# Optimization experiments

Hardware: AMD Instinct MI355X
Metric: run time of the kernel (lower is better)

Reference implementation:

```python
import jax, jax.numpy as jnp
import numpy as np

B, T, IN_CH, FIRST_CH, BLOCK_CH, SCALED_CH, K, ND = 8, 16384, 256, 256, 24, 128, 2, 10


def _conv1d(x, W, b, d=1):
    # x: (B, L, Cin), W: (K, Cin, Cout), keras Conv1D with padding='valid'
    y = jax.lax.conv_general_dilated(x, W, (1,), 'VALID', rhs_dilation=(d,),
                                     dimension_numbers=('NWC', 'WIO', 'NWC'))
    return y + b


def _gated(x, gW, gb, fW, fb, sW, sb, d):
    g = jax.nn.sigmoid(_conv1d(x, gW, gb, d))
    f = jnp.tanh(_conv1d(x, fW, fb, d))
    return _conv1d(f * g, sW, sb, 1)


def setup_inputs():
    key = jax.random.key(0)
    ks = jax.random.split(key, 11)
    s = 0.1
    n9 = ND - 1  # blocks 1..9 share channel count BLOCK_CH -> stacked weights
    return {
        'x': jax.random.normal(ks[0], (B, T, IN_CH), jnp.float32),
        'causal_W': jax.random.normal(ks[1], (K, IN_CH, FIRST_CH)) * s,
        'causal_b': jnp.zeros((FIRST_CH,)),
        'gW0': jax.random.normal(ks[2], (K, FIRST_CH, BLOCK_CH)) * s,
        'gb0': jnp.zeros((BLOCK_CH,)),
        'fW0': jax.random.normal(ks[3], (K, FIRST_CH, BLOCK_CH)) * s,
        'fb0': jnp.zeros((BLOCK_CH,)),
        'sW0': jax.random.normal(ks[4], (1, BLOCK_CH, BLOCK_CH)) * s,
        'sb0': jnp.zeros((BLOCK_CH,)),
        'gate_W': jax.random.normal(ks[5], (n9, K, BLOCK_CH, BLOCK_CH)) * s,
        'gate_b': jnp.zeros((n9, BLOCK_CH)),
        'filter_W': jax.random.normal(ks[6], (n9, K, BLOCK_CH, BLOCK_CH)) * s,
        'filter_b': jnp.zeros((n9, BLOCK_CH)),
        'scale_W': jax.random.normal(ks[7], (n9, 1, BLOCK_CH, BLOCK_CH)) * s,
        'scale_b': jnp.zeros((n9, BLOCK_CH)),
        'res_W': jax.random.normal(ks[8], (n9, 1, BLOCK_CH, SCALED_CH)) * s,
        'res_b': jnp.zeros((n9, SCALED_CH)),
        'f1_W': jax.random.normal(ks[9], (1, SCALED_CH, IN_CH)) * s,
        'f1_b': jnp.zeros((IN_CH,)),
        'f2_W': jax.random.normal(ks[10], (1, IN_CH, IN_CH)) * s,
        'f2_b': jnp.zeros((IN_CH,)),
    }


def reference(x, causal_W, causal_b, gW0, gb0, fW0, fb0, sW0, sb0,
              gate_W, gate_b, filter_W, filter_b, scale_W, scale_b,
              res_W, res_b, f1_W, f1_b, f2_W, f2_b):
    out = _conv1d(x, causal_W, causal_b)  # (B, T-1, 256)
    # block 0 (dilation 1): prev_in has 256 ch vs 24 ch out -> residual branch skipped
    out = _gated(out, gW0, gb0, fW0, fb0, sW0, sb0, 1)
    acc = None
    for i in range(ND - 1):
        d = 2 ** (i + 1)  # even -> trim d//2 on each side
        prev = out
        out = _gated(prev, gate_W[i], gate_b[i], filter_W[i], filter_b[i],
                     scale_W[i], scale_b[i], d)
        trimmed = prev[:, d // 2: prev.shape[1] - d // 2, :]
        # NOTE: original code OVERWRITES the accumulator each iteration
        acc = _conv1d(trimmed + out, res_W[i], res_b[i], 1)
    a = jax.nn.relu(acc)  # (B, 15360, 128)
    a = jax.nn.relu(_conv1d(a, f1_W, f1_b, 1))  # (B, 15360, 256)
    return jax.nn.softmax(_conv1d(a, f2_W, f2_b, 1), axis=-1)
```

## Files before the change

kernel.cpp:

```cpp
#include <hip/hip_runtime.h>
#include <math.h>

typedef unsigned short u16;
typedef __attribute__((ext_vector_type(8))) short short8;
typedef __attribute__((ext_vector_type(4))) float f32x4;

#define PBSTR ((long)16382 * 24)

__device__ __forceinline__ u16 f2bf(float f) {
    unsigned u = __float_as_uint(f);
    unsigned r = u + 0x7FFFu + ((u >> 16) & 1u);
    return (u16)(r >> 16);
}
__device__ __forceinline__ float bf2f(u16 v) { return __uint_as_float((unsigned)v << 16); }
__device__ __forceinline__ float sigf(float x) { return 1.f / (1.f + __expf(-x)); }
__device__ __forceinline__ float tanhfast(float x) { return 2.f / (1.f + __expf(-2.f * x)) - 1.f; }

__device__ __forceinline__ unsigned cvtpk(float a, float b) {
    unsigned r;
    asm("v_cvt_pk_bf16_f32 %0, %1, %2" : "=v"(r) : "v"(a), "v"(b));
    return r;
}
__device__ __forceinline__ short8 ldfrag8(const float* p) {
    float4 v0 = *(const float4*)p;
    float4 v1 = *(const float4*)(p + 4);
    union { uint4 u; short8 s; } cv;
    cv.u.x = cvtpk(v0.x, v0.y); cv.u.y = cvtpk(v0.z, v0.w);
    cv.u.z = cvtpk(v1.x, v1.y); cv.u.w = cvtpk(v1.z, v1.w);
    return cv.s;
}

__global__ __launch_bounds__(256) void build_all(
    const float* __restrict__ cW, const float* __restrict__ cb,
    const float* __restrict__ gW, const float* __restrict__ gb,
    const float* __restrict__ fW, const float* __restrict__ fb,
    u16* __restrict__ Wt, float* __restrict__ biasGF,
    const float* __restrict__ f1W, const float* __restrict__ f2W,
    const float* __restrict__ resW8,
    const float* __restrict__ gateW, const float* __restrict__ filtW,
    const float* __restrict__ sclW, const float* __restrict__ s0W,
    u16* __restrict__ Wt1, u16* __restrict__ Wt2, u16* __restrict__ Wtr,
    u16* __restrict__ Wgf, u16* __restrict__ Wsc)
{
    if (blockIdx.x < 192) {
        int idx = blockIdx.x * 256 + threadIdx.x;
        if (idx < 49152) {
            int nr = idx / 768, k = idx % 768, tau = k / 256, ci = k % 256;
            float val = 0.f;
            if (nr < 48) {
                const float* G = (nr < 24) ? gW : fW;
                int n = (nr < 24) ? nr : nr - 24;
                auto dotf = [&](int i, int j) {
                    const float* a = cW + i * 65536 + ci * 256;
                    const float* g = G + j * 6144 + n;
                    float s = 0.f;
                    for (int o = 0; o < 256; o += 4) {
                        float4 av = *(const float4*)(a + o);
                        const float* gp = g + o * 24;
                        s += av.x * gp[0] + av.y * gp[24] + av.z * gp[48] + av.w * gp[72];
                    }
                    return s;
                };
                if (tau == 0)      val = dotf(0, 0);
                else if (tau == 1) val = dotf(0, 1) + dotf(1, 0);
                else               val = dotf(1, 1);
            }
            Wt[idx] = f2bf(val);
        }
        if (blockIdx.x == 0 && threadIdx.x < 48) {
            int nr = threadIdx.x;
            const float* G = (nr < 24) ? gW : fW;
            const float* B = (nr < 24) ? gb : fb;
            int n = (nr < 24) ? nr : nr - 24;
            float s = B[n];
            for (int o = 0; o < 256; ++o) s += cb[o] * (G[o * 24 + n] + G[6144 + o * 24 + n]);
            biasGF[nr] = s;
        }
    } else {
        int idx = (blockIdx.x - 192) * 256 + threadIdx.x;
        if (idx < 32768) {
            int n = idx / 128, k = idx % 128;
            Wt1[idx] = f2bf(f1W[k * 256 + n]);
        } else if (idx < 98304) {
            int j = idx - 32768; int n = j / 256, k = j % 256;
            Wt2[j] = f2bf(f2W[k * 256 + n]);
        } else if (idx < 102400) {
            int j = idx - 98304; int n = j / 32, k = j % 32;
            Wtr[j] = (k < 24) ? f2bf(resW8[k * 128 + n]) : (u16)0;
        } else if (idx < 130048) {
            int j = idx - 102400;
            int i = j / 3072, r = (j % 3072) / 64, k = j % 64;
            float v = 0.f;
            int tap = -1, ci = 0;
            if (k < 24) { tap = 0; ci = k; }
            else if (k >= 32 && k < 56) { tap = 1; ci = k - 32; }
            if (tap >= 0) {
                const float* W = (r < 24) ? gateW : filtW;
                int co = (r < 24) ? r : r - 24;
                v = W[((i * 2 + tap) * 24 + ci) * 24 + co];
            }
            Wgf[j] = f2bf(v);
        } else if (idx < 140288) {
            int j = idx - 130048;
            int i = j / 1024, r = (j % 1024) / 32, k = j % 32;
            const float* S = (i < 9) ? (sclW + (size_t)i * 576) : s0W;
            float v = (r < 24 && k < 24) ? S[k * 24 + r] : 0.f;
            Wsc[j] = f2bf(v);
        }
    }
}

__global__ __launch_bounds__(256) void gf_fused_v6(
    const float* __restrict__ x, const u16* __restrict__ Wt,
    const float* __restrict__ biasGF,
    const u16* __restrict__ ws0, const float* __restrict__ sb,
    u16* __restrict__ P)
{
    __shared__ __align__(16) union {
        u16 bs[48 * 776];
        u16 H[256 * 40];
    } U;

    const int tid = threadIdx.x;
    const int m0 = blockIdx.x * 256;
    const int b = blockIdx.z;
    const float* xb = x + (long)b * (16384 * 256);

    for (int i = tid; i < 4608; i += 256) {
        int rn = i / 96, kk = i % 96;
        *(uint4*)&U.bs[rn * 776 + kk * 8] = *(const uint4*)(Wt + (long)rn * 768 + kk * 8);
    }

    const int wv = tid >> 6, lane = tid & 63, col = lane & 15, quad = lane >> 4;

    short8 wsf0 = *(const short8*)(ws0 + col * 32 + quad * 8);
    short8 wsf1 = *(const short8*)(ws0 + (16 + col) * 32 + quad * 8);
    const float bv0 = biasGF[col];
    const float bv1 = (col < 8) ? biasGF[16 + col] : biasGF[24 + col - 8];
    const float bv2 = biasGF[32 + col];
    const float sv0 = sb[col];
    const float sv1 = (col < 8) ? sb[16 + col] : 0.f;

    long rowoff[4];
#pragma unroll
    for (int mt = 0; mt < 4; ++mt) {
        int g = m0 + wv * 64 + mt * 16 + col;
        if (g > 16381) g = 16381;
        rowoff[mt] = (long)g * 256 + quad * 8;
    }

    f32x4 acc[4][3];
#pragma unroll
    for (int i = 0; i < 4; ++i)
#pragma unroll
        for (int j = 0; j < 3; ++j) acc[i][j] = (f32x4){0.f, 0.f, 0.f, 0.f};

    __syncthreads();

    for (int s = 0; s < 24; ++s) {
        short8 a[4];
#pragma unroll
        for (int mt = 0; mt < 4; ++mt)
            a[mt] = ldfrag8(xb + rowoff[mt] + s * 32);
#pragma unroll
        for (int nt = 0; nt < 3; ++nt) {
            short8 bb = *(const short8*)&U.bs[(nt * 16 + col) * 776 + s * 32 + quad * 8];
#pragma unroll
            for (int mt = 0; mt < 4; ++mt)
                acc[mt][nt] = __builtin_amdgcn_mfma_f32_16x16x32_bf16(a[mt], bb, acc[mt][nt], 0, 0, 0);
        }
    }

    __syncthreads();
    *(uint4*)&U.H[tid * 40 + 24] = (uint4){0, 0, 0, 0};

#pragma unroll
    for (int mt = 0; mt < 4; ++mt) {
        const int lr = wv * 64 + mt * 16 + quad * 4;
#pragma unroll
        for (int rr = 0; rr < 4; ++rr) {
            float g0 = acc[mt][0][rr] + bv0;
            float m1 = acc[mt][1][rr] + bv1;
            float m2 = acc[mt][2][rr] + bv2;
            float s1 = __shfl_xor(m1, 8);
            float s2 = __shfl_xor(m2, 8);
            float f0 = (col < 8) ? s1 : s2;
            U.H[(lr + rr) * 40 + col] = f2bf(sigf(g0) * tanhfast(f0));
            if (col < 8)
                U.H[(lr + rr) * 40 + 16 + col] = f2bf(sigf(m1) * tanhfast(s2));
        }
    }
    __syncthreads();

#pragma unroll
    for (int mt = 0; mt < 4; ++mt) {
        short8 aH = *(const short8*)&U.H[(wv * 64 + mt * 16 + col) * 40 + quad * 8];
        f32x4 c0 = {0.f, 0.f, 0.f, 0.f}, c1 = c0;
        c0 = __builtin_amdgcn_mfma_f32_16x16x32_bf16(aH, wsf0, c0, 0, 0, 0);
        c1 = __builtin_amdgcn_mfma_f32_16x16x32_bf16(aH, wsf1, c1, 0, 0, 0);
#pragma unroll
        for (int rr = 0; rr < 4; ++rr) {
            int t = m0 + wv * 64 + mt * 16 + quad * 4 + rr;
            if (t < 16382) {
                P[(long)b * PBSTR + (long)t * 24 + col] = f2bf(c0[rr] + sv0);
                if (col < 8)
                    P[(long)b * PBSTR + (long)t * 24 + 16 + col] = f2bf(c1[rr] + sv1);
            }
        }
    }
}

__global__ __launch_bounds__(256) void gated_mfma_v3(
    const u16* __restrict__ Pin,
    const u16* __restrict__ wg,
    const u16* __restrict__ ws,
    const float* __restrict__ gB, const float* __restrict__ fB,
    const float* __restrict__ sB,
    u16* __restrict__ Q, int Lout, int d, int trimOff)
{
    __shared__ __align__(16) u16 T[128 * 72];
    __shared__ __align__(16) u16 H[128 * 40];

    const int tid = threadIdx.x;
    const int wv = tid >> 6, lane = tid & 63, col = lane & 15, quad = lane >> 4;
    const int m0 = blockIdx.x * 128;
    const int b = blockIdx.z;
    const u16* Pb = Pin + (long)b * PBSTR;

    {
        int r = tid & 127, tap = tid >> 7;
        int t = m0 + r; if (t > Lout - 1) t = Lout - 1;
        const u16* src = Pb + (long)(t + tap * d) * 24;
        u16* dst = &T[r * 72 + tap * 32];
        *(uint4*)(dst)      = *(const uint4*)(src);
        *(uint4*)(dst + 8)  = *(const uint4*)(src + 8);
        *(uint4*)(dst + 16) = *(const uint4*)(src + 16);
        *(uint4*)(dst + 24) = (uint4){0, 0, 0, 0};
    }
    if (tid < 128) *(uint4*)&H[tid * 40 + 24] = (uint4){0, 0, 0, 0};

    short8 bgf0[3], bgf1[3];
#pragma unroll
    for (int nt = 0; nt < 3; ++nt) {
        bgf0[nt] = *(const short8*)(wg + (nt * 16 + col) * 64 + quad * 8);
        bgf1[nt] = *(const short8*)(wg + (nt * 16 + col) * 64 + 32 + quad * 8);
    }
    short8 wsf0 = *(const short8*)(ws + col * 32 + quad * 8);
    short8 wsf1 = *(const short8*)(ws + (16 + col) * 32 + quad * 8);
    const float bv0 = gB[col];
    const float bv1 = (col < 8) ? gB[16 + col] : fB[col - 8];
    const float bv2 = fB[8 + col];
    const float sv0 = sB[col];
    const float sv1 = (col < 8) ? sB[16 + col] : 0.f;

    __syncthreads();

#pragma unroll
    for (int mt = 0; mt < 2; ++mt) {
        const int r = wv * 32 + mt * 16;
        short8 a0 = *(const short8*)&T[(r + col) * 72 + quad * 8];
        short8 a1 = *(const short8*)&T[(r + col) * 72 + 32 + quad * 8];
        f32x4 ac0 = {0.f, 0.f, 0.f, 0.f}, ac1 = ac0, ac2 = ac0;
        ac0 = __builtin_amdgcn_mfma_f32_16x16x32_bf16(a0, bgf0[0], ac0, 0, 0, 0);
        ac0 = __builtin_amdgcn_mfma_f32_16x16x32_bf16(a1, bgf1[0], ac0, 0, 0, 0);
        ac1 = __builtin_amdgcn_mfma_f32_16x16x32_bf16(a0, bgf0[1], ac1, 0, 0, 0);
        ac1 = __builtin_amdgcn_mfma_f32_16x16x32_bf16(a1, bgf1[1], ac1, 0, 0, 0);
        ac2 = __builtin_amdgcn_mfma_f32_16x16x32_bf16(a0, bgf0[2], ac2, 0, 0, 0);
        ac2 = __builtin_amdgcn_mfma_f32_16x16x32_bf16(a1, bgf1[2], ac2, 0, 0, 0);

        const int lr = r + quad * 4;
#pragma unroll
        for (int rr = 0; rr < 4; ++rr) {
            float g0 = ac0[rr] + bv0;
            float m1 = ac1[rr] + bv1;
            float m2 = ac2[rr] + bv2;
            float s1 = __shfl_xor(m1, 8);
            float s2 = __shfl_xor(m2, 8);
            float f0 = (col < 8) ? s1 : s2;
            H[(lr + rr) * 40 + col] = f2bf(sigf(g0) * tanhfast(f0));
            if (col < 8)
                H[(lr + rr) * 40 + 16 + col] = f2bf(sigf(m1) * tanhfast(s2));
        }
    }
    __syncthreads();

#pragma unroll
    for (int mt = 0; mt < 2; ++mt) {
        short8 aH = *(const short8*)&H[(wv * 32 + mt * 16 + col) * 40 + quad * 8];
        f32x4 c0 = {0.f, 0.f, 0.f, 0.f}, c1 = c0;
        c0 = __builtin_amdgcn_mfma_f32_16x16x32_bf16(aH, wsf0, c0, 0, 0, 0);
        c1 = __builtin_amdgcn_mfma_f32_16x16x32_bf16(aH, wsf1, c1, 0, 0, 0);
#pragma unroll
        for (int rr = 0; rr < 4; ++rr) {
            int t = m0 + wv * 32 + mt * 16 + quad * 4 + rr;
            if (t < Lout) {
                float v0 = c0[rr] + sv0;
                if (trimOff >= 0) v0 += bf2f(Pb[(long)(t + trimOff) * 24 + col]);
                Q[(long)b * PBSTR + (long)t * 24 + col] = f2bf(v0);
                if (col < 8) {
                    float v1 = c1[rr] + sv1;
                    if (trimOff >= 0) v1 += bf2f(Pb[(long)(t + trimOff) * 24 + 16 + col]);
                    Q[(long)b * PBSTR + (long)t * 24 + 16 + col] = f2bf(v1);
                }
            }
        }
    }
}

__global__ __launch_bounds__(256) void res_f1_fused(
    const u16* __restrict__ Pfin,
    const u16* __restrict__ Wtr, const float* __restrict__ resb,
    const u16* __restrict__ Wt1, const float* __restrict__ f1b,
    u16* __restrict__ A1)
{
    __shared__ __align__(16) u16 ACCs[128 * 136];
    __shared__ __align__(16) u16 W1s[128 * 136];
    __shared__ float biasL[128];

    const int tid = threadIdx.x;
    const int wv = tid >> 6, lane = tid & 63, col = lane & 15, quad = lane >> 4;
    const int b = blockIdx.z;
    const int n0 = blockIdx.y * 128;
    const int m0 = blockIdx.x * 128;
    const u16* Pb = Pfin + (long)b * PBSTR;

    for (int i = tid; i < 2048; i += 256) {
        int rn = i >> 4, kk = i & 15;
        *(uint4*)&W1s[rn * 136 + kk * 8] = *(const uint4*)(Wt1 + (long)(n0 + rn) * 128 + kk * 8);
    }
    if (tid < 128) biasL[tid] = f1b[n0 + tid];

    short8 bfr[8];
    float rbv[8];
#pragma unroll
    for (int nt = 0; nt < 8; ++nt) {
        bfr[nt] = *(const short8*)(Wtr + (nt * 16 + col) * 32 + quad * 8);
        rbv[nt] = resb[nt * 16 + col];
    }
    short8 afr[2];
#pragma unroll
    for (int mt = 0; mt < 2; ++mt) {
        int r = m0 + wv * 32 + mt * 16 + col;
        if (r > 15359) r = 15359;
        afr[mt] = *(const short8*)(Pb + (long)r * 24 + quad * 8);
    }
    f32x4 acc[2][8];
#pragma unroll
    for (int i = 0; i < 2; ++i)
#pragma unroll
        for (int j = 0; j < 8; ++j) acc[i][j] = (f32x4){0.f, 0.f, 0.f, 0.f};
#pragma unroll
    for (int nt = 0; nt < 8; ++nt) {
        acc[0][nt] = __builtin_amdgcn_mfma_f32_16x16x32_bf16(afr[0], bfr[nt], acc[0][nt], 0, 0, 0);
        acc[1][nt] = __builtin_amdgcn_mfma_f32_16x16x32_bf16(afr[1], bfr[nt], acc[1][nt], 0, 0, 0);
    }
#pragma unroll
    for (int mt = 0; mt < 2; ++mt)
#pragma unroll
        for (int nt = 0; nt < 8; ++nt)
#pragma unroll
            for (int rr = 0; rr < 4; ++rr) {
                int lrow = wv * 32 + mt * 16 + quad * 4 + rr;
                ACCs[lrow * 136 + nt * 16 + col] = f2bf(fmaxf(acc[mt][nt][rr] + rbv[nt], 0.f));
            }
    __syncthreads();

    f32x4 acc2[2][8];
#pragma unroll
    for (int i = 0; i < 2; ++i)
#pragma unroll
        for (int j = 0; j < 8; ++j) acc2[i][j] = (f32x4){0.f, 0.f, 0.f, 0.f};
#pragma unroll
    for (int ks = 0; ks < 4; ++ks) {
        short8 am[2];
#pragma unroll
        for (int mt = 0; mt < 2; ++mt)
            am[mt] = *(const short8*)&ACCs[(wv * 32 + mt * 16 + col) * 136 + ks * 32 + quad * 8];
#pragma unroll
        for (int nt = 0; nt < 8; ++nt) {
            short8 bb = *(const short8*)&W1s[(nt * 16 + col) * 136 + ks * 32 + quad * 8];
            acc2[0][nt] = __builtin_amdgcn_mfma_f32_16x16x32_bf16(am[0], bb, acc2[0][nt], 0, 0, 0);
            acc2[1][nt] = __builtin_amdgcn_mfma_f32_16x16x32_bf16(am[1], bb, acc2[1][nt], 0, 0, 0);
        }
    }
#pragma unroll
    for (int mt = 0; mt < 2; ++mt)
#pragma unroll
        for (int nt = 0; nt < 8; ++nt)
#pragma unroll
            for (int rr = 0; rr < 4; ++rr) {
                int t = m0 + wv * 32 + mt * 16 + quad * 4 + rr;
                float v = fmaxf(acc2[mt][nt][rr] + biasL[nt * 16 + col], 0.f);
                A1[((long)b * 15360 + t) * 256 + n0 + nt * 16 + col] = f2bf(v);
            }
}

__global__ __launch_bounds__(256) void f2_softmax_v2(
    const u16* __restrict__ A, const u16* __restrict__ Wt2,
    const float* __restrict__ bias, float* __restrict__ out)
{
    __shared__ __align__(16) u16 Bs[2][256 * 40];
    __shared__ float biasL[256];
    const int tid = threadIdx.x;
    const int b = blockIdx.y;
    const int t0 = blockIdx.x * 64;
    biasL[tid] = bias[tid];

    const int wv = tid >> 6, lane = tid & 63, col = lane & 15, quad = lane >> 4;
    const u16* Ab = A + (long)b * (15360L * 256);
    const int row = t0 + wv * 16 + col;

    auto stage = [&](int kc, int buf) {
#pragma unroll
        for (int j = 0; j < 4; ++j) {
            int idx = tid * 4 + j;
            int rn = idx >> 2, kk = idx & 3;
            *(uint4*)&Bs[buf][rn * 40 + kk * 8] =
                *(const uint4*)(Wt2 + (long)rn * 256 + kc * 32 + kk * 8);
        }
    };

    short8 afr[8];
#pragma unroll
    for (int kc = 0; kc < 8; ++kc)
        afr[kc] = *(const short8*)(Ab + (long)row * 256 + kc * 32 + quad * 8);

    f32x4 acc[16];
#pragma unroll
    for (int i = 0; i < 16; ++i) acc[i] = (f32x4){0.f, 0.f, 0.f, 0.f};

    stage(0, 0);
    __syncthreads();
    for (int kc = 0; kc < 8; ++kc) {
        int buf = kc & 1;
        if (kc < 7) stage(kc + 1, buf ^ 1);
#pragma unroll
        for (int nt = 0; nt < 16; ++nt) {
            short8 bb = *(const short8*)&Bs[buf][(nt * 16 + col) * 40 + quad * 8];
            acc[nt] = __builtin_amdgcn_mfma_f32_16x16x32_bf16(afr[kc], bb, acc[nt], 0, 0, 0);
        }
        __syncthreads();
    }

#pragma unroll
    for (int r = 0; r < 4; ++r) {
        int tl = wv * 16 + quad * 4 + r;
        float v[16];
        float m = -1e30f;
#pragma unroll
        for (int nt = 0; nt < 16; ++nt) {
            v[nt] = acc[nt][r] + biasL[nt * 16 + col];
            m = fmaxf(m, v[nt]);
        }
        m = fmaxf(m, __shfl_xor(m, 1));
        m = fmaxf(m, __shfl_xor(m, 2));
        m = fmaxf(m, __shfl_xor(m, 4));
        m = fmaxf(m, __shfl_xor(m, 8));
        float s = 0.f;
#pragma unroll
        for (int nt = 0; nt < 16; ++nt) { v[nt] = __expf(v[nt] - m); s += v[nt]; }
        s += __shfl_xor(s, 1);
        s += __shfl_xor(s, 2);
        s += __shfl_xor(s, 4);
        s += __shfl_xor(s, 8);
        float inv = 1.f / s;
        float* op = out + ((long)b * 15360 + t0 + tl) * 256;
#pragma unroll
        for (int nt = 0; nt < 16; ++nt) op[nt * 16 + col] = v[nt] * inv;
    }
}

extern "C" void kernel_launch(void* const* d_in, const int* in_sizes, int n_in,
                              void* d_out, int out_size, void* d_ws, size_t ws_size,
                              hipStream_t stream)
{
    const float* x        = (const float*)d_in[0];
    const float* causal_W = (const float*)d_in[1];
    const float* causal_b = (const float*)d_in[2];
    const float* gW0      = (const float*)d_in[3];
    const float* gb0      = (const float*)d_in[4];
    const float* fW0      = (const float*)d_in[5];
    const float* fb0      = (const float*)d_in[6];
    const float* sW0      = (const float*)d_in[7];
    const float* sb0      = (const float*)d_in[8];
    const float* gate_W   = (const float*)d_in[9];
    const float* gate_b   = (const float*)d_in[10];
    const float* filter_W = (const float*)d_in[11];
    const float* filter_b = (const float*)d_in[12];
    const float* scale_W  = (const float*)d_in[13];
    const float* scale_b  = (const float*)d_in[14];
    const float* res_W    = (const float*)d_in[15];
    const float* res_b    = (const float*)d_in[16];
    const float* f1_W     = (const float*)d_in[17];
    const float* f1_b     = (const float*)d_in[18];
    const float* f2_W     = (const float*)d_in[19];
    const float* f2_b     = (const float*)d_in[20];

    char* w = (char*)d_ws;
    u16* A1   = (u16*)w;   w += (size_t)8 * 15360 * 256 * 2;
    u16* P0   = (u16*)w;   w += (size_t)8 * 16382 * 24 * 2 + 128;
    u16* P1   = (u16*)w;   w += (size_t)8 * 16382 * 24 * 2 + 128;
    u16* WtGF = (u16*)w;   w += (size_t)64 * 768 * 2;
    u16* Wt1  = (u16*)w;   w += (size_t)256 * 128 * 2;
    u16* Wt2  = (u16*)w;   w += (size_t)256 * 256 * 2;
    u16* Wtr  = (u16*)w;   w += (size_t)128 * 32 * 2;
    float* biasGF = (float*)w; w += 256;
    u16* WgfG = (u16*)w;   w += (size_t)9 * 48 * 64 * 2;
    u16* WsG  = (u16*)w;   w += (size_t)10 * 32 * 32 * 2;

    dim3 blk(256);

    build_all<<<dim3(740), blk, 0, stream>>>(
        causal_W, causal_b, gW0, gb0, fW0, fb0, WtGF, biasGF,
        f1_W, f2_W, res_W + (size_t)8 * 24 * 128,
        gate_W, filter_W, scale_W, sW0,
        Wt1, Wt2, Wtr, WgfG, WsG);

    gf_fused_v6<<<dim3(64, 1, 8), blk, 0, stream>>>(
        x, WtGF, biasGF, WsG + (size_t)9 * 1024, sb0, P0);

    u16* Pprev = P0;
    u16* Pnext = P1;
    int Lprev = 16382;
    for (int i = 0; i < 9; ++i) {
        int d = 2 << i;
        int L = Lprev - d;
        int trim = (i == 8) ? d / 2 : -1;
        gated_mfma_v3<<<dim3((L + 127) / 128, 1, 8), blk, 0, stream>>>(
            Pprev, WgfG + (size_t)i * 3072, WsG + (size_t)i * 1024,
            gate_b + i * 24, filter_b + i * 24, scale_b + i * 24,
            Pnext, L, d, trim);
        u16* tmp = Pprev; Pprev = Pnext; Pnext = tmp;
        Lprev = L;
    }

    res_f1_fused<<<dim3(120, 2, 8), blk, 0, stream>>>(
        Pprev, Wtr, res_b + 8 * 128, Wt1, f1_b, A1);

    f2_softmax_v2<<<dim3(240, 8), blk, 0, stream>>>(A1, Wt2, f2_b, (float*)d_out);
}
```

Before: 546.7 us.

## Double-buffer x tiles into LDS via async global_load_lds in first fused kernel

The first fused conv+gated kernel now stages 128-row fp32 x tiles into LDS with asynchronous global_load_lds, double-buffered and XOR-swizzled, instead of each lane loading its A fragments straight from global memory. The block tile is halved from 256 to 128 rows, doubling the grid, and the weight slab is loaded in two halves to shrink LDS. The aim is to overlap the large x read with MFMA work and raise occupancy. In exchange it adds a barrier per K step and a mid-loop weight reload, and each row's data is now fetched through LDS rather than held in registers.

```diff
diff --git a/kernel.cpp b/kernel.cpp
--- a/kernel.cpp
+++ b/kernel.cpp
@@ -28,6 +28,12 @@
     cv.u.x = cvtpk(v0.x, v0.y); cv.u.y = cvtpk(v0.z, v0.w);
     cv.u.z = cvtpk(v1.x, v1.y); cv.u.w = cvtpk(v1.z, v1.w);
     return cv.s;
+}
+
+__device__ __forceinline__ void gload16(const float* g, float* l) {
+    __builtin_amdgcn_global_load_lds(
+        (const __attribute__((address_space(1))) unsigned int*)g,
+        (__attribute__((address_space(3))) unsigned int*)l, 16, 0, 0);
 }
 
 __global__ __launch_bounds__(256) void build_all(
@@ -110,28 +116,45 @@
     }
 }
 
-__global__ __launch_bounds__(256) void gf_fused_v6(
+__global__ __launch_bounds__(256) void gf_fused_v7(
     const float* __restrict__ x, const u16* __restrict__ Wt,
     const float* __restrict__ biasGF,
     const u16* __restrict__ ws0, const float* __restrict__ sb,
     u16* __restrict__ P)
 {
     __shared__ __align__(16) union {
-        u16 bs[48 * 776];
-        u16 H[256 * 40];
+        u16 bs[48 * 392];
+        u16 H[128 * 40];
     } U;
+    __shared__ __align__(16) float ab[2][128 * 32];
 
     const int tid = threadIdx.x;
-    const int m0 = blockIdx.x * 256;
+    const int wv = tid >> 6, lane = tid & 63, col = lane & 15, quad = lane >> 4;
+    const int m0 = blockIdx.x * 128;
     const int b = blockIdx.z;
     const float* xb = x + (long)b * (16384 * 256);
 
-    for (int i = tid; i < 4608; i += 256) {
-        int rn = i / 96, kk = i % 96;
-        *(uint4*)&U.bs[rn * 776 + kk * 8] = *(const uint4*)(Wt + (long)rn * 768 + kk * 8);
-    }
-
-    const int wv = tid >> 6, lane = tid & 63, col = lane & 15, quad = lane >> 4;
+    long srcoff[4];
+#pragma unroll
+    for (int j = 0; j < 4; ++j) {
+        int lin = j * 256 + tid;
+        int rl = lin >> 3;
+        int r = m0 + rl;
+        if (r > 16381) r = 16381;
+        int ii = (lin & 7) ^ (rl & 7);
+        srcoff[j] = (long)r * 256 + ii * 4;
+    }
+
+    auto stageA = [&](int ks, int bufi) {
+#pragma unroll
+        for (int j = 0; j < 4; ++j)
+            gload16(xb + srcoff[j] + ks * 32, &ab[bufi][j * 1024 + wv * 256]);
+    };
+
+    for (int i = tid; i < 2304; i += 256) {
+        int rn = i / 48, kk = i % 48;
+        *(uint4*)&U.bs[rn * 392 + kk * 8] = *(const uint4*)(Wt + (long)rn * 768 + kk * 8);
+    }
 
     short8 wsf0 = *(const short8*)(ws0 + col * 32 + quad * 8);
     short8 wsf1 = *(const short8*)(ws0 + (16 + col) * 32 + quad * 8);
@@ -141,42 +164,55 @@
     const float sv0 = sb[col];
     const float sv1 = (col < 8) ? sb[16 + col] : 0.f;
 
-    long rowoff[4];
-#pragma unroll
-    for (int mt = 0; mt < 4; ++mt) {
-        int g = m0 + wv * 64 + mt * 16 + col;
-        if (g > 16381) g = 16381;
-        rowoff[mt] = (long)g * 256 + quad * 8;
-    }
-
-    f32x4 acc[4][3];
-#pragma unroll
-    for (int i = 0; i < 4; ++i)
+    f32x4 acc[2][3];
+#pragma unroll
+    for (int i = 0; i < 2; ++i)
 #pragma unroll
         for (int j = 0; j < 3; ++j) acc[i][j] = (f32x4){0.f, 0.f, 0.f, 0.f};
 
+    stageA(0, 0);
     __syncthreads();
 
-    for (int s = 0; s < 24; ++s) {
-        short8 a[4];
-#pragma unroll
-        for (int mt = 0; mt < 4; ++mt)
-            a[mt] = ldfrag8(xb + rowoff[mt] + s * 32);
+    for (int ks = 0; ks < 24; ++ks) {
+        if (ks < 23) stageA(ks + 1, (ks + 1) & 1);
+        if (ks == 12) {
+            for (int i = tid; i < 2304; i += 256) {
+                int rn = i / 48, kk = i % 48;
+                *(uint4*)&U.bs[rn * 392 + kk * 8] =
+                    *(const uint4*)(Wt + (long)rn * 768 + 384 + kk * 8);
+            }
+            __syncthreads();
+        }
+        const int cur = ks & 1;
+        const int kb = (ks % 12) * 32;
+
+        short8 a[2];
+#pragma unroll
+        for (int mt = 0; mt < 2; ++mt) {
+            const int row = wv * 32 + mt * 16 + col;
+            const int sw = row & 7;
+            const float* base = &ab[cur][row * 32];
+            float4 v0 = *(const float4*)(base + ((2 * quad) ^ sw) * 4);
+            float4 v1 = *(const float4*)(base + ((2 * quad + 1) ^ sw) * 4);
+            union { uint4 u; short8 s8; } cv;
+            cv.u.x = cvtpk(v0.x, v0.y); cv.u.y = cvtpk(v0.z, v0.w);
+            cv.u.z = cvtpk(v1.x, v1.y); cv.u.w = cvtpk(v1.z, v1.w);
+            a[mt] = cv.s8;
+        }
 #pragma unroll
         for (int nt = 0; nt < 3; ++nt) {
-            short8 bb = *(const short8*)&U.bs[(nt * 16 + col) * 776 + s * 32 + quad * 8];
-#pragma unroll
-            for (int mt = 0; mt < 4; ++mt)
-                acc[mt][nt] = __builtin_amdgcn_mfma_f32_16x16x32_bf16(a[mt], bb, acc[mt][nt], 0, 0, 0);
-        }
-    }
-
-    __syncthreads();
-    *(uint4*)&U.H[tid * 40 + 24] = (uint4){0, 0, 0, 0};
-
-#pragma unroll
-    for (int mt = 0; mt < 4; ++mt) {
-        const int lr = wv * 64 + mt * 16 + quad * 4;
+            short8 bb = *(const short8*)&U.bs[(nt * 16 + col) * 392 + kb + quad * 8];
+            acc[0][nt] = __builtin_amdgcn_mfma_f32_16x16x32_bf16(a[0], bb, acc[0][nt], 0, 0, 0);
+            acc[1][nt] = __builtin_amdgcn_mfma_f32_16x16x32_bf16(a[1], bb, acc[1][nt], 0, 0, 0);
+        }
+        __syncthreads();
+    }
+
+    if (tid < 128) *(uint4*)&U.H[tid * 40 + 24] = (uint4){0, 0, 0, 0};
+
+#pragma unroll
+    for (int mt = 0; mt < 2; ++mt) {
+        const int lr = wv * 32 + mt * 16 + quad * 4;
 #pragma unroll
         for (int rr = 0; rr < 4; ++rr) {
             float g0 = acc[mt][0][rr] + bv0;
@@ -193,14 +229,14 @@
     __syncthreads();
 
 #pragma unroll
-    for (int mt = 0; mt < 4; ++mt) {
-        short8 aH = *(const short8*)&U.H[(wv * 64 + mt * 16 + col) * 40 + quad * 8];
+    for (int mt = 0; mt < 2; ++mt) {
+        short8 aH = *(const short8*)&U.H[(wv * 32 + mt * 16 + col) * 40 + quad * 8];
         f32x4 c0 = {0.f, 0.f, 0.f, 0.f}, c1 = c0;
         c0 = __builtin_amdgcn_mfma_f32_16x16x32_bf16(aH, wsf0, c0, 0, 0, 0);
         c1 = __builtin_amdgcn_mfma_f32_16x16x32_bf16(aH, wsf1, c1, 0, 0, 0);
 #pragma unroll
         for (int rr = 0; rr < 4; ++rr) {
-            int t = m0 + wv * 64 + mt * 16 + quad * 4 + rr;
+            int t = m0 + wv * 32 + mt * 16 + quad * 4 + rr;
             if (t < 16382) {
                 P[(long)b * PBSTR + (long)t * 24 + col] = f2bf(c0[rr] + sv0);
                 if (col < 8)
@@ -516,7 +552,7 @@
         gate_W, filter_W, scale_W, sW0,
         Wt1, Wt2, Wtr, WgfG, WsG);
 
-    gf_fused_v6<<<dim3(64, 1, 8), blk, 0, stream>>>(
+    gf_fused_v7<<<dim3(128, 1, 8), blk, 0, stream>>>(
         x, WtGF, biasGF, WsG + (size_t)9 * 1024, sb0, P0);
 
     u16* Pprev = P0;
```

Result: no change. 544.5 us (-0.4%).

## Stage x tile as bf16 in swizzled LDS and shrink gf block to 64 rows

Applied to the files above, without the earlier changes.

The first fused gated kernel now stages its 64-row x tile into shared memory as bf16 with an XOR swizzle, instead of loading fp32 fragments straight from global memory inside the MFMA loop. Block size drops from 256 to 64 rows (grid 64 to 256 blocks per batch), and the weight tile is loaded in two K halves to fit LDS. The aim is more parallelism (512 to 2048 blocks total), coalesced global loads and less register pressure. The cost is that each block now loads the weights twice, plus extra barriers.

```diff
diff --git a/kernel.cpp b/kernel.cpp
--- a/kernel.cpp
+++ b/kernel.cpp
@@ -20,14 +20,6 @@
     unsigned r;
     asm("v_cvt_pk_bf16_f32 %0, %1, %2" : "=v"(r) : "v"(a), "v"(b));
     return r;
-}
-__device__ __forceinline__ short8 ldfrag8(const float* p) {
-    float4 v0 = *(const float4*)p;
-    float4 v1 = *(const float4*)(p + 4);
-    union { uint4 u; short8 s; } cv;
-    cv.u.x = cvtpk(v0.x, v0.y); cv.u.y = cvtpk(v0.z, v0.w);
-    cv.u.z = cvtpk(v1.x, v1.y); cv.u.w = cvtpk(v1.z, v1.w);
-    return cv.s;
 }
 
 __global__ __launch_bounds__(256) void build_all(
@@ -110,28 +102,39 @@
     }
 }
 
-__global__ __launch_bounds__(256) void gf_fused_v6(
+__global__ __launch_bounds__(256) void gf_fused_v8(
     const float* __restrict__ x, const u16* __restrict__ Wt,
     const float* __restrict__ biasGF,
     const u16* __restrict__ ws0, const float* __restrict__ sb,
     u16* __restrict__ P)
 {
     __shared__ __align__(16) union {
-        u16 bs[48 * 776];
-        u16 H[256 * 40];
+        u16 bs[48 * 392];
+        u16 H[64 * 40];
     } U;
+    __shared__ __align__(16) u16 A[64 * 256];
 
     const int tid = threadIdx.x;
-    const int m0 = blockIdx.x * 256;
+    const int wv = tid >> 6, lane = tid & 63, col = lane & 15, quad = lane >> 4;
+    const int m0 = blockIdx.x * 64;
     const int b = blockIdx.z;
     const float* xb = x + (long)b * (16384 * 256);
 
-    for (int i = tid; i < 4608; i += 256) {
-        int rn = i / 96, kk = i % 96;
-        *(uint4*)&U.bs[rn * 776 + kk * 8] = *(const uint4*)(Wt + (long)rn * 768 + kk * 8);
-    }
-
-    const int wv = tid >> 6, lane = tid & 63, col = lane & 15, quad = lane >> 4;
+    for (int i = tid; i < 2304; i += 256) {
+        int rn = i / 48, kk = i % 48;
+        *(uint4*)&U.bs[rn * 392 + kk * 8] = *(const uint4*)(Wt + (long)rn * 768 + kk * 8);
+    }
+
+#pragma unroll
+    for (int j = 0; j < 16; ++j) {
+        int lin = j * 256 + tid;
+        int rl = lin >> 6, c = lin & 63;
+        int r = m0 + rl; if (r > 16381) r = 16381;
+        float4 v = *(const float4*)(xb + (long)r * 256 + c * 4);
+        uint2 w2;
+        w2.x = cvtpk(v.x, v.y); w2.y = cvtpk(v.z, v.w);
+        *(uint2*)&A[rl * 256 + (c ^ ((rl & 7) << 1)) * 4] = w2;
+    }
 
     short8 wsf0 = *(const short8*)(ws0 + col * 32 + quad * 8);
     short8 wsf1 = *(const short8*)(ws0 + (16 + col) * 32 + quad * 8);
@@ -141,47 +144,47 @@
     const float sv0 = sb[col];
     const float sv1 = (col < 8) ? sb[16 + col] : 0.f;
 
-    long rowoff[4];
-#pragma unroll
-    for (int mt = 0; mt < 4; ++mt) {
-        int g = m0 + wv * 64 + mt * 16 + col;
-        if (g > 16381) g = 16381;
-        rowoff[mt] = (long)g * 256 + quad * 8;
-    }
-
-    f32x4 acc[4][3];
-#pragma unroll
-    for (int i = 0; i < 4; ++i)
-#pragma unroll
-        for (int j = 0; j < 3; ++j) acc[i][j] = (f32x4){0.f, 0.f, 0.f, 0.f};
-
-    __syncthreads();
-
-    for (int s = 0; s < 24; ++s) {
-        short8 a[4];
-#pragma unroll
-        for (int mt = 0; mt < 4; ++mt)
-            a[mt] = ldfrag8(xb + rowoff[mt] + s * 32);
-#pragma unroll
-        for (int nt = 0; nt < 3; ++nt) {
-            short8 bb = *(const short8*)&U.bs[(nt * 16 + col) * 776 + s * 32 + quad * 8];
-#pragma unroll
-            for (int mt = 0; mt < 4; ++mt)
-                acc[mt][nt] = __builtin_amdgcn_mfma_f32_16x16x32_bf16(a[mt], bb, acc[mt][nt], 0, 0, 0);
-        }
-    }
-
-    __syncthreads();
-    *(uint4*)&U.H[tid * 40 + 24] = (uint4){0, 0, 0, 0};
-
-#pragma unroll
-    for (int mt = 0; mt < 4; ++mt) {
-        const int lr = wv * 64 + mt * 16 + quad * 4;
+    f32x4 acc[3];
+#pragma unroll
+    for (int j = 0; j < 3; ++j) acc[j] = (f32x4){0.f, 0.f, 0.f, 0.f};
+
+    const int arow = wv * 16 + col;
+    const int asw = arow & 7;
+    __syncthreads();
+
+#pragma unroll
+    for (int half = 0; half < 2; ++half) {
+        if (half) {
+            __syncthreads();
+            for (int i = tid; i < 2304; i += 256) {
+                int rn = i / 48, kk = i % 48;
+                *(uint4*)&U.bs[rn * 392 + kk * 8] =
+                    *(const uint4*)(Wt + (long)rn * 768 + 384 + kk * 8);
+            }
+            __syncthreads();
+        }
+#pragma unroll
+        for (int s = 0; s < 12; ++s) {
+            const int ks = half * 12 + s;
+            short8 a = *(const short8*)&A[arow * 256 + (((ks * 4 + quad) ^ asw) << 3)];
+#pragma unroll
+            for (int nt = 0; nt < 3; ++nt) {
+                short8 bb = *(const short8*)&U.bs[(nt * 16 + col) * 392 + s * 32 + quad * 8];
+                acc[nt] = __builtin_amdgcn_mfma_f32_16x16x32_bf16(a, bb, acc[nt], 0, 0, 0);
+            }
+        }
+    }
+
+    __syncthreads();
+    if (tid < 64) *(uint4*)&U.H[tid * 40 + 24] = (uint4){0, 0, 0, 0};
+
+    {
+        const int lr = wv * 16 + quad * 4;
 #pragma unroll
         for (int rr = 0; rr < 4; ++rr) {
-            float g0 = acc[mt][0][rr] + bv0;
-            float m1 = acc[mt][1][rr] + bv1;
-            float m2 = acc[mt][2][rr] + bv2;
+            float g0 = acc[0][rr] + bv0;
+            float m1 = acc[1][rr] + bv1;
+            float m2 = acc[2][rr] + bv2;
             float s1 = __shfl_xor(m1, 8);
             float s2 = __shfl_xor(m2, 8);
             float f0 = (col < 8) ? s1 : s2;
@@ -192,15 +195,14 @@
     }
     __syncthreads();
 
-#pragma unroll
-    for (int mt = 0; mt < 4; ++mt) {
-        short8 aH = *(const short8*)&U.H[(wv * 64 + mt * 16 + col) * 40 + quad * 8];
+    {
+        short8 aH = *(const short8*)&U.H[(wv * 16 + col) * 40 + quad * 8];
         f32x4 c0 = {0.f, 0.f, 0.f, 0.f}, c1 = c0;
         c0 = __builtin_amdgcn_mfma_f32_16x16x32_bf16(aH, wsf0, c0, 0, 0, 0);
         c1 = __builtin_amdgcn_mfma_f32_16x16x32_bf16(aH, wsf1, c1, 0, 0, 0);
 #pragma unroll
         for (int rr = 0; rr < 4; ++rr) {
-            int t = m0 + wv * 64 + mt * 16 + quad * 4 + rr;
+            int t = m0 + wv * 16 + quad * 4 + rr;
             if (t < 16382) {
                 P[(long)b * PBSTR + (long)t * 24 + col] = f2bf(c0[rr] + sv0);
                 if (col < 8)
@@ -516,7 +518,7 @@
         gate_W, filter_W, scale_W, sW0,
         Wt1, Wt2, Wtr, WgfG, WsG);
 
-    gf_fused_v6<<<dim3(64, 1, 8), blk, 0, stream>>>(
+    gf_fused_v8<<<dim3(256, 1, 8), blk, 0, stream>>>(
         x, WtGF, biasGF, WsG + (size_t)9 * 1024, sb0, P0);
 
     u16* Pprev = P0;
```

After: 515.1 us. 1.06x faster.
